# Performance work log

Measured on AMD Instinct MI355X. Metric: run time of the kernel, lower is better.

The kernel has to match this reference:

```python
import jax, jax.numpy as jnp
import numpy as np
from functools import partial

SEQ, BATCH, IN, HID = 512, 128, 256, 1024


def setup_inputs() -> dict:
    key = jax.random.key(0)
    ks = jax.random.split(key, 8)
    std = 1.0 / np.sqrt(HID)
    u = lambda k, shape: jax.random.uniform(k, shape, jnp.float32, -std, std)
    return {
        "inp": jax.random.normal(ks[0], (SEQ, BATCH, IN), jnp.float32),
        "Wxh": u(ks[1], (4 * HID, IN)),
        "bxh": u(ks[2], (4 * HID,)),
        "Whh": u(ks[3], (4 * HID, HID)),
        "bhh": u(ks[4], (4 * HID,)),
        "Wout": u(ks[5], (IN, HID)),
        "bout": u(ks[6], (IN,)),
    }


def lstm_forward(inp, Wxh, bxh, Whh, bhh, Wout, bout):
    seq, batch, _ = inp.shape
    hid = Whh.shape[1]
    # Precompute input projection for all timesteps: [T, B, 4H]
    x_proj = jnp.einsum("tbi,gi->tbg", inp, Wxh) + bxh

    def step(carry, xp_t):
        h, c = carry
        gates = xp_t + h @ Whh.T + bhh            # [B, 4H]
        i, f, g, o = jnp.split(gates, 4, axis=-1)  # torch chunk order: i,f,g,o
        c = jax.nn.sigmoid(f) * c + jax.nn.sigmoid(i) * jnp.tanh(g)
        h = jax.nn.sigmoid(o) * jnp.tanh(c)
        return (h, c), h

    h0 = jnp.zeros((batch, hid), inp.dtype)
    c0 = jnp.zeros((batch, hid), inp.dtype)
    _, hs = jax.lax.scan(step, (h0, c0), x_proj)   # hs: [T, B, H]
    out = jnp.einsum("tbh,ih->tbi", hs, Wout) + bout
    return jax.nn.log_softmax(out, axis=-1)


def reference(inp, Wxh, bxh, Whh, bhh, Wout, bout):
    return lstm_forward(inp, Wxh, bxh, Whh, bhh, Wout, bout)
```

## Files before the change

kernel.cpp:

```cpp
#include <hip/hip_runtime.h>
#include <math.h>


#define TT  512
#define BB  128
#define NIN 256
#define NH  1024
#define G4  4096
#define KK  1280

typedef __bf16 bf16_t;
typedef bf16_t bf16x8 __attribute__((ext_vector_type(8)));
typedef float  f32x4  __attribute__((ext_vector_type(4)));

#define MFMA(a, b, c) __builtin_amdgcn_mfma_f32_16x16x32_bf16((a), (b), (c), 0, 0, 0)


__global__ void conv_w_kernel(const float* __restrict__ Wxh,
                              const float* __restrict__ Whh,
                              bf16_t* __restrict__ Wc) {
  const int n = blockIdx.y;
  const int k = blockIdx.x * 256 + threadIdx.x;
  const int g = n & 3, j = n >> 2;
  float v = (k < NIN) ? Wxh[(size_t)(g * NH + j) * NIN + k]
                      : Whh[(size_t)(g * NH + j) * NH + (k - NIN)];
  Wc[(size_t)n * KK + k] = (bf16_t)v;
}

__global__ void conv_f2b_kernel(const float* __restrict__ src,
                                bf16_t* __restrict__ dst, int n4) {
  int i = blockIdx.x * 256 + threadIdx.x;
  if (i < n4) {
    float4 v = ((const float4*)src)[i];
    dst[i * 4 + 0] = (bf16_t)v.x;
    dst[i * 4 + 1] = (bf16_t)v.y;
    dst[i * 4 + 2] = (bf16_t)v.z;
    dst[i * 4 + 3] = (bf16_t)v.w;
  }
}

__global__ void prep_bias_kernel(const float* __restrict__ bxh,
                                 const float* __restrict__ bhh,
                                 float* __restrict__ bsum4) {
  int n = blockIdx.x * 256 + threadIdx.x;
  int g = n & 3, j = n >> 2;
  bsum4[n] = bxh[g * NH + j] + bhh[g * NH + j];
}


__global__ __launch_bounds__(256) void fused_step(
    int t,
    const bf16_t* __restrict__ x_bf,
    const bf16_t* __restrict__ Wc,
    const float*  __restrict__ bsum4,
    const bf16_t* __restrict__ h_cur,
    bf16_t*       __restrict__ h_next,
    float*        __restrict__ c,
    const bf16_t* __restrict__ WoutB,
    const float*  __restrict__ bout,
    float*        __restrict__ logits_w,
    const float*  __restrict__ logits_r,
    float*        __restrict__ out)
{
  const int blk  = blockIdx.x;
  const int tid  = threadIdx.x;
  const int lane = tid & 63;
  const int wv   = tid >> 6;
  const int l16  = lane & 15;
  const int lq   = lane >> 4;

  if (blk < 128) {
    if (t >= TT) return;
    __shared__ float gs[64 * 68];

    const int mb    = (blk & 1) * 64;
    const int ns    = blk >> 1;
    const int nbase = ns * 64;
    const int wm = wv & 1, wn = wv >> 1;
    const int m0 = mb + wm * 32;
    const int n0 = nbase + wn * 32;

    const bf16_t* ax  = x_bf + (size_t)t * BB * NIN + (size_t)(m0 + l16) * NIN + lq * 8;
    const bf16_t* ah  = h_cur + (size_t)(m0 + l16) * NH + lq * 8;
    const bf16_t* b0p = Wc + (size_t)(n0 + l16) * KK + lq * 8;
    const bf16_t* b1p = Wc + (size_t)(n0 + 16 + l16) * KK + lq * 8;

    f32x4 a00 = {0,0,0,0}, a01 = {0,0,0,0}, a10 = {0,0,0,0}, a11 = {0,0,0,0};

#pragma unroll
    for (int kk = 0; kk < 8; ++kk) {
      bf16x8 r0 = *(const bf16x8*)(ax + kk * 32);
      bf16x8 r1 = *(const bf16x8*)(ax + 16 * NIN + kk * 32);
      bf16x8 b0 = *(const bf16x8*)(b0p + kk * 32);
      bf16x8 b1 = *(const bf16x8*)(b1p + kk * 32);
      a00 = MFMA(r0, b0, a00); a01 = MFMA(r0, b1, a01);
      a10 = MFMA(r1, b0, a10); a11 = MFMA(r1, b1, a11);
    }
#pragma unroll 8
    for (int kk = 0; kk < 32; ++kk) {
      bf16x8 r0 = *(const bf16x8*)(ah + kk * 32);
      bf16x8 r1 = *(const bf16x8*)(ah + 16 * NH + kk * 32);
      bf16x8 b0 = *(const bf16x8*)(b0p + NIN + kk * 32);
      bf16x8 b1 = *(const bf16x8*)(b1p + NIN + kk * 32);
      a00 = MFMA(r0, b0, a00); a01 = MFMA(r0, b1, a01);
      a10 = MFMA(r1, b0, a10); a11 = MFMA(r1, b1, a11);
    }

#pragma unroll
    for (int r = 0; r < 4; ++r) {
      const int rr0 = wm * 32 + lq * 4 + r;
      gs[rr0 * 68 + wn * 32 + l16]             = a00[r];
      gs[rr0 * 68 + wn * 32 + 16 + l16]        = a01[r];
      gs[(rr0 + 16) * 68 + wn * 32 + l16]      = a10[r];
      gs[(rr0 + 16) * 68 + wn * 32 + 16 + l16] = a11[r];
    }
    __syncthreads();

    const int b_l = tid >> 2;
#pragma unroll
    for (int p = 0; p < 4; ++p) {
      const int jl = (tid & 3) + p * 4;
      const int j  = ns * 16 + jl;
      float4 g4 = *(const float4*)&gs[b_l * 68 + jl * 4];
      float4 bs = ((const float4*)bsum4)[j];
      const float gi = g4.x + bs.x;
      const float gf = g4.y + bs.y;
      const float gg = g4.z + bs.z;
      const float go = g4.w + bs.w;
      const float si = 1.f / (1.f + __expf(-gi));
      const float sf = 1.f / (1.f + __expf(-gf));
      const float so = 1.f / (1.f + __expf(-go));
      const size_t idx = (size_t)(mb + b_l) * NH + j;
      const float cn = sf * c[idx] + si * tanhf(gg);
      c[idx] = cn;
      h_next[idx] = (bf16_t)(so * tanhf(cn));
    }
  } else if (blk < 160) {
    if (t < 1 || t > TT) return;
    const int gw  = (blk - 128) * 4 + wv;
    const int bm0 = (gw >> 4) * 16;
    const int bn0 = (gw & 15) * 16;

    const bf16_t* ap = h_cur + (size_t)(bm0 + l16) * NH + lq * 8;
    const bf16_t* bp = WoutB + (size_t)(bn0 + l16) * NH + lq * 8;
    f32x4 acc = {0,0,0,0};
#pragma unroll 8
    for (int kk = 0; kk < 32; ++kk) {
      bf16x8 a = *(const bf16x8*)(ap + kk * 32);
      bf16x8 b = *(const bf16x8*)(bp + kk * 32);
      acc = MFMA(a, b, acc);
    }
    const float bo = bout[bn0 + l16];
#pragma unroll
    for (int r = 0; r < 4; ++r)
      logits_w[(size_t)(bm0 + lq * 4 + r) * NIN + bn0 + l16] = acc[r] + bo;
  } else {
    if (t < 2) return;
    __shared__ float red[2][4][4];
    const int b0 = (blk - 160) * 4;
    float v[4], mx[4], sm[4];
#pragma unroll
    for (int r = 0; r < 4; ++r) v[r] = logits_r[(size_t)(b0 + r) * NIN + tid];
#pragma unroll
    for (int r = 0; r < 4; ++r) mx[r] = v[r];
#pragma unroll
    for (int off = 32; off > 0; off >>= 1)
#pragma unroll
      for (int r = 0; r < 4; ++r) mx[r] = fmaxf(mx[r], __shfl_xor(mx[r], off));
    if (lane == 0)
#pragma unroll
      for (int r = 0; r < 4; ++r) red[0][wv][r] = mx[r];
    __syncthreads();
#pragma unroll
    for (int r = 0; r < 4; ++r)
      mx[r] = fmaxf(fmaxf(red[0][0][r], red[0][1][r]),
                    fmaxf(red[0][2][r], red[0][3][r]));
#pragma unroll
    for (int r = 0; r < 4; ++r) sm[r] = __expf(v[r] - mx[r]);
#pragma unroll
    for (int off = 32; off > 0; off >>= 1)
#pragma unroll
      for (int r = 0; r < 4; ++r) sm[r] += __shfl_xor(sm[r], off);
    if (lane == 0)
#pragma unroll
      for (int r = 0; r < 4; ++r) red[1][wv][r] = sm[r];
    __syncthreads();
    float* ot = out + (size_t)(t - 2) * BB * NIN + (size_t)b0 * NIN;
#pragma unroll
    for (int r = 0; r < 4; ++r) {
      float S = red[1][0][r] + red[1][1][r] + red[1][2][r] + red[1][3][r];
      ot[(size_t)r * NIN + tid] = v[r] - mx[r] - logf(S);
    }
  }
}


extern "C" void kernel_launch(void* const* d_in, const int* in_sizes, int n_in,
                              void* d_out, int out_size, void* d_ws, size_t ws_size,
                              hipStream_t stream) {
  const float* inp  = (const float*)d_in[0];
  const float* Wxh  = (const float*)d_in[1];
  const float* bxh  = (const float*)d_in[2];
  const float* Whh  = (const float*)d_in[3];
  const float* bhh  = (const float*)d_in[4];
  const float* Wout = (const float*)d_in[5];
  const float* bout = (const float*)d_in[6];
  float* out = (float*)d_out;

  char* p = (char*)d_ws;
  bf16_t* Wc    = (bf16_t*)p; p += (size_t)G4 * KK * 2;
  bf16_t* x_bf  = (bf16_t*)p; p += (size_t)TT * BB * NIN * 2;
  bf16_t* WoutB = (bf16_t*)p; p += (size_t)NIN * NH * 2;
  bf16_t* h0    = (bf16_t*)p; p += (size_t)BB * NH * 2;
  bf16_t* h1    = (bf16_t*)p; p += (size_t)BB * NH * 2;
  float*  cbuf  = (float*)p;  p += (size_t)BB * NH * 4;
  float*  bsum4 = (float*)p;  p += (size_t)G4 * 4;
  float*  lg0   = (float*)p;  p += (size_t)BB * NIN * 4;
  float*  lg1   = (float*)p;  p += (size_t)BB * NIN * 4;

  conv_w_kernel<<<dim3(KK / 256, G4), 256, 0, stream>>>(Wxh, Whh, Wc);
  conv_f2b_kernel<<<(TT * BB * NIN / 4 + 255) / 256, 256, 0, stream>>>(
      inp, x_bf, TT * BB * NIN / 4);
  conv_f2b_kernel<<<(NIN * NH / 4 + 255) / 256, 256, 0, stream>>>(
      Wout, WoutB, NIN * NH / 4);
  prep_bias_kernel<<<G4 / 256, 256, 0, stream>>>(bxh, bhh, bsum4);
  hipMemsetAsync(h0, 0, (size_t)BB * NH * 2, stream);
  hipMemsetAsync(cbuf, 0, (size_t)BB * NH * 4, stream);

  bf16_t* hb[2] = {h0, h1};
  float*  lg[2] = {lg0, lg1};
  for (int t = 0; t < TT + 2; ++t) {
    fused_step<<<192, 256, 0, stream>>>(
        t, x_bf, Wc, bsum4,
        hb[t & 1], hb[(t + 1) & 1], cbuf,
        WoutB, bout,
        lg[t & 1],
        lg[(t + 1) & 1],
        out);
  }
}
```

Baseline: 11.15 ms.

## Split LSTM step GEMM across K with 512-thread blocks and merge output stages

Each gate block now computes a 64x32 tile, and its eight waves split the K dimension four ways. Partial sums go through shared memory and are added up before the gate nonlinearities. The launch grows to 256 blocks of 512 threads, so more CUs and waves share each per-step recurrent GEMM, which shortens the serial critical path. The output projection and log-softmax now run on the first 32 gate blocks instead of separate blocks, and the softmax becomes one wave per row with float4 loads. The cost is extra shared-memory reduction traffic and a heavier tail in the blocks that carry the extra work.

```diff
diff --git a/kernel.cpp b/kernel.cpp
--- a/kernel.cpp
+++ b/kernel.cpp
@@ -48,7 +48,7 @@
 }
 
 
-__global__ __launch_bounds__(256) void fused_step(
+__global__ __launch_bounds__(512, 2) void fused_step(
     int t,
     const bf16_t* __restrict__ x_bf,
     const bf16_t* __restrict__ Wc,
@@ -69,127 +69,110 @@
   const int l16  = lane & 15;
   const int lq   = lane >> 4;
 
-  if (blk < 128) {
-    if (t >= TT) return;
-    __shared__ float gs[64 * 68];
-
+  __shared__ float gs[4 * 64 * 36];
+
+  if (t < TT) {
     const int mb    = (blk & 1) * 64;
     const int ns    = blk >> 1;
-    const int nbase = ns * 64;
-    const int wm = wv & 1, wn = wv >> 1;
+    const int nbase = ns * 32;
+    const int wm = wv & 1;
+    const int wk = wv >> 1;
     const int m0 = mb + wm * 32;
-    const int n0 = nbase + wn * 32;
 
     const bf16_t* ax  = x_bf + (size_t)t * BB * NIN + (size_t)(m0 + l16) * NIN + lq * 8;
     const bf16_t* ah  = h_cur + (size_t)(m0 + l16) * NH + lq * 8;
-    const bf16_t* b0p = Wc + (size_t)(n0 + l16) * KK + lq * 8;
-    const bf16_t* b1p = Wc + (size_t)(n0 + 16 + l16) * KK + lq * 8;
+    const bf16_t* b0p = Wc + (size_t)(nbase + l16) * KK + lq * 8;
+    const bf16_t* b1p = b0p + (size_t)16 * KK;
 
     f32x4 a00 = {0,0,0,0}, a01 = {0,0,0,0}, a10 = {0,0,0,0}, a11 = {0,0,0,0};
 
-#pragma unroll
-    for (int kk = 0; kk < 8; ++kk) {
-      bf16x8 r0 = *(const bf16x8*)(ax + kk * 32);
-      bf16x8 r1 = *(const bf16x8*)(ax + 16 * NIN + kk * 32);
-      bf16x8 b0 = *(const bf16x8*)(b0p + kk * 32);
-      bf16x8 b1 = *(const bf16x8*)(b1p + kk * 32);
+    const int xo = wk * 64;
+#pragma unroll
+    for (int i = 0; i < 2; ++i) {
+      const int off = xo + i * 32;
+      bf16x8 r0 = *(const bf16x8*)(ax + off);
+      bf16x8 r1 = *(const bf16x8*)(ax + 16 * NIN + off);
+      bf16x8 b0 = *(const bf16x8*)(b0p + off);
+      bf16x8 b1 = *(const bf16x8*)(b1p + off);
       a00 = MFMA(r0, b0, a00); a01 = MFMA(r0, b1, a01);
       a10 = MFMA(r1, b0, a10); a11 = MFMA(r1, b1, a11);
     }
-#pragma unroll 8
-    for (int kk = 0; kk < 32; ++kk) {
-      bf16x8 r0 = *(const bf16x8*)(ah + kk * 32);
-      bf16x8 r1 = *(const bf16x8*)(ah + 16 * NH + kk * 32);
-      bf16x8 b0 = *(const bf16x8*)(b0p + NIN + kk * 32);
-      bf16x8 b1 = *(const bf16x8*)(b1p + NIN + kk * 32);
+    const int ho = wk * 256;
+#pragma unroll
+    for (int i = 0; i < 8; ++i) {
+      const int off = ho + i * 32;
+      bf16x8 r0 = *(const bf16x8*)(ah + off);
+      bf16x8 r1 = *(const bf16x8*)(ah + 16 * NH + off);
+      bf16x8 b0 = *(const bf16x8*)(b0p + NIN + off);
+      bf16x8 b1 = *(const bf16x8*)(b1p + NIN + off);
       a00 = MFMA(r0, b0, a00); a01 = MFMA(r0, b1, a01);
       a10 = MFMA(r1, b0, a10); a11 = MFMA(r1, b1, a11);
     }
 
+    float* gr = gs + wk * (64 * 36);
 #pragma unroll
     for (int r = 0; r < 4; ++r) {
-      const int rr0 = wm * 32 + lq * 4 + r;
-      gs[rr0 * 68 + wn * 32 + l16]             = a00[r];
-      gs[rr0 * 68 + wn * 32 + 16 + l16]        = a01[r];
-      gs[(rr0 + 16) * 68 + wn * 32 + l16]      = a10[r];
-      gs[(rr0 + 16) * 68 + wn * 32 + 16 + l16] = a11[r];
+      const int rr = wm * 32 + lq * 4 + r;
+      gr[rr * 36 + l16]             = a00[r];
+      gr[rr * 36 + 16 + l16]        = a01[r];
+      gr[(rr + 16) * 36 + l16]      = a10[r];
+      gr[(rr + 16) * 36 + 16 + l16] = a11[r];
     }
     __syncthreads();
 
-    const int b_l = tid >> 2;
-#pragma unroll
-    for (int p = 0; p < 4; ++p) {
-      const int jl = (tid & 3) + p * 4;
-      const int j  = ns * 16 + jl;
-      float4 g4 = *(const float4*)&gs[b_l * 68 + jl * 4];
-      float4 bs = ((const float4*)bsum4)[j];
-      const float gi = g4.x + bs.x;
-      const float gf = g4.y + bs.y;
-      const float gg = g4.z + bs.z;
-      const float go = g4.w + bs.w;
-      const float si = 1.f / (1.f + __expf(-gi));
-      const float sf = 1.f / (1.f + __expf(-gf));
-      const float so = 1.f / (1.f + __expf(-go));
-      const size_t idx = (size_t)(mb + b_l) * NH + j;
-      const float cn = sf * c[idx] + si * tanhf(gg);
-      c[idx] = cn;
-      h_next[idx] = (bf16_t)(so * tanhf(cn));
-    }
-  } else if (blk < 160) {
-    if (t < 1 || t > TT) return;
-    const int gw  = (blk - 128) * 4 + wv;
-    const int bm0 = (gw >> 4) * 16;
-    const int bn0 = (gw & 15) * 16;
-
-    const bf16_t* ap = h_cur + (size_t)(bm0 + l16) * NH + lq * 8;
-    const bf16_t* bp = WoutB + (size_t)(bn0 + l16) * NH + lq * 8;
-    f32x4 acc = {0,0,0,0};
+    const int b_l = tid >> 3;
+    const int jl  = tid & 7;
+    const int j   = ns * 8 + jl;
+    const float4 g0 = *(const float4*)&gs[0 * 64 * 36 + b_l * 36 + jl * 4];
+    const float4 g1 = *(const float4*)&gs[1 * 64 * 36 + b_l * 36 + jl * 4];
+    const float4 g2 = *(const float4*)&gs[2 * 64 * 36 + b_l * 36 + jl * 4];
+    const float4 g3 = *(const float4*)&gs[3 * 64 * 36 + b_l * 36 + jl * 4];
+    const float4 bs = ((const float4*)bsum4)[j];
+    const float gi = g0.x + g1.x + g2.x + g3.x + bs.x;
+    const float gf = g0.y + g1.y + g2.y + g3.y + bs.y;
+    const float gg = g0.z + g1.z + g2.z + g3.z + bs.z;
+    const float go = g0.w + g1.w + g2.w + g3.w + bs.w;
+    const float si = 1.f / (1.f + __expf(-gi));
+    const float sf = 1.f / (1.f + __expf(-gf));
+    const float so = 1.f / (1.f + __expf(-go));
+    const size_t idx = (size_t)(mb + b_l) * NH + j;
+    const float cn = sf * c[idx] + si * tanhf(gg);
+    c[idx] = cn;
+    h_next[idx] = (bf16_t)(so * tanhf(cn));
+  }
+
+  if (blk < 16) {
+    if (t >= 1 && t <= TT) {
+      const int gw  = blk * 8 + wv;
+      const int bm0 = (gw >> 4) * 16;
+      const int bn0 = (gw & 15) * 16;
+      const bf16_t* ap = h_cur + (size_t)(bm0 + l16) * NH + lq * 8;
+      const bf16_t* bp = WoutB + (size_t)(bn0 + l16) * NH + lq * 8;
+      f32x4 acc = {0,0,0,0};
 #pragma unroll 8
-    for (int kk = 0; kk < 32; ++kk) {
-      bf16x8 a = *(const bf16x8*)(ap + kk * 32);
-      bf16x8 b = *(const bf16x8*)(bp + kk * 32);
-      acc = MFMA(a, b, acc);
-    }
-    const float bo = bout[bn0 + l16];
-#pragma unroll
-    for (int r = 0; r < 4; ++r)
-      logits_w[(size_t)(bm0 + lq * 4 + r) * NIN + bn0 + l16] = acc[r] + bo;
-  } else {
-    if (t < 2) return;
-    __shared__ float red[2][4][4];
-    const int b0 = (blk - 160) * 4;
-    float v[4], mx[4], sm[4];
-#pragma unroll
-    for (int r = 0; r < 4; ++r) v[r] = logits_r[(size_t)(b0 + r) * NIN + tid];
-#pragma unroll
-    for (int r = 0; r < 4; ++r) mx[r] = v[r];
-#pragma unroll
-    for (int off = 32; off > 0; off >>= 1)
-#pragma unroll
-      for (int r = 0; r < 4; ++r) mx[r] = fmaxf(mx[r], __shfl_xor(mx[r], off));
-    if (lane == 0)
-#pragma unroll
-      for (int r = 0; r < 4; ++r) red[0][wv][r] = mx[r];
-    __syncthreads();
-#pragma unroll
-    for (int r = 0; r < 4; ++r)
-      mx[r] = fmaxf(fmaxf(red[0][0][r], red[0][1][r]),
-                    fmaxf(red[0][2][r], red[0][3][r]));
-#pragma unroll
-    for (int r = 0; r < 4; ++r) sm[r] = __expf(v[r] - mx[r]);
-#pragma unroll
-    for (int off = 32; off > 0; off >>= 1)
-#pragma unroll
-      for (int r = 0; r < 4; ++r) sm[r] += __shfl_xor(sm[r], off);
-    if (lane == 0)
-#pragma unroll
-      for (int r = 0; r < 4; ++r) red[1][wv][r] = sm[r];
-    __syncthreads();
-    float* ot = out + (size_t)(t - 2) * BB * NIN + (size_t)b0 * NIN;
-#pragma unroll
-    for (int r = 0; r < 4; ++r) {
-      float S = red[1][0][r] + red[1][1][r] + red[1][2][r] + red[1][3][r];
-      ot[(size_t)r * NIN + tid] = v[r] - mx[r] - logf(S);
+      for (int kk = 0; kk < 32; ++kk) {
+        bf16x8 a = *(const bf16x8*)(ap + kk * 32);
+        bf16x8 b = *(const bf16x8*)(bp + kk * 32);
+        acc = MFMA(a, b, acc);
+      }
+      const float bo = bout[bn0 + l16];
+#pragma unroll
+      for (int r = 0; r < 4; ++r)
+        logits_w[(size_t)(bm0 + lq * 4 + r) * NIN + bn0 + l16] = acc[r] + bo;
+    }
+  } else if (blk < 32) {
+    if (t >= 2) {
+      const int rr = (blk - 16) * 8 + wv;
+      float4 v = ((const float4*)(logits_r + (size_t)rr * NIN))[lane];
+      float m = fmaxf(fmaxf(v.x, v.y), fmaxf(v.z, v.w));
+#pragma unroll
+      for (int off = 32; off > 0; off >>= 1) m = fmaxf(m, __shfl_xor(m, off));
+      float s = __expf(v.x - m) + __expf(v.y - m) + __expf(v.z - m) + __expf(v.w - m);
+#pragma unroll
+      for (int off = 32; off > 0; off >>= 1) s += __shfl_xor(s, off);
+      const float lse = m + logf(s);
+      float4 o = make_float4(v.x - lse, v.y - lse, v.z - lse, v.w - lse);
+      ((float4*)(out + (size_t)(t - 2) * BB * NIN + (size_t)rr * NIN))[lane] = o;
     }
   }
 }
@@ -230,7 +213,7 @@
   bf16_t* hb[2] = {h0, h1};
   float*  lg[2] = {lg0, lg1};
   for (int t = 0; t < TT + 2; ++t) {
-    fused_step<<<192, 256, 0, stream>>>(
+    fused_step<<<256, 512, 0, stream>>>(
         t, x_bf, Wc, bsum4,
         hb[t & 1], hb[(t + 1) & 1], cbuf,
         WoutB, bout,
```

Result: slower. 13.68 ms (+22.7%).
